# Kernel tuning notes

Measured on AMD Instinct MI355X. Metric: run time of the kernel, lower is better.

The kernel has to match this reference:

```python
import jax, jax.numpy as jnp
import numpy as np

N, C, H, W = 16, 64, 128, 128
SHIFT = 1  # frozen value of torch module's random.randint(-2, 2) drawn at __init__


def setup_inputs() -> dict:
    key = jax.random.key(0)
    k1, k2, k3 = jax.random.split(key, 3)
    x = jax.random.normal(k1, (N, C, H, W), dtype=jnp.float32)
    # p_3: Conv2d(c, c, (1,5), padding=(0,2), bias=False) -> weight (C_out, C_in, 1, 5)
    w3 = jax.random.normal(k2, (C, C, 1, 5), dtype=jnp.float32) * (1.0 / np.sqrt(5.0 * C))
    # p_7: Conv2d(9c, c, 1, groups=c, bias=False) -> per output channel, 9 input channels: (C, 9)
    w7 = jax.random.normal(k3, (C, 9), dtype=jnp.float32) * (1.0 / 3.0)
    return {"x": x, "w3": w3, "w7": w7}


def reference(x, w3, w7):
    n, c, h, w = x.shape
    # t_1: F.unfold(x, (1,3), dilation=(1,2), padding=(0,2)) -> width offsets -2, 0, +2 (zero padded)
    xp = jnp.pad(x, ((0, 0), (0, 0), (0, 0), (2, 2)))
    t1 = jnp.stack([xp[..., 0:w], xp[..., 2:w + 2], xp[..., 4:w + 4]], axis=2)  # (n,c,3,h,w)
    # t_3: 1x5 conv, padding (0,2)
    t3 = jax.lax.conv_general_dilated(
        x, w3, window_strides=(1, 1), padding=[(0, 0), (2, 2)],
        dimension_numbers=("NCHW", "OIHW", "NCHW"))  # (n,c,h,w)
    # t_4: F.unfold(t1 as (n,3c,h,w), (3,1), padding=(1,0)) -> height offsets -1, 0, +1
    t1p = jnp.pad(t1, ((0, 0), (0, 0), (0, 0), (1, 1), (0, 0)))
    t4 = jnp.stack([t1p[..., 0:h, :], t1p[..., 1:h + 1, :], t1p[..., 2:h + 2, :]],
                   axis=3)  # (n, c, 3[w_off], 3[h_off], h, w)
    # t_5: roll along the W axis (dim 5)
    t5 = jnp.roll(t4, SHIFT, axis=5)
    # t_6: maximum of lhs (n,c,1,3,h,w) and rhs (n,c,3,3,h,w); lhs offset dim aligns with rhs dim 3
    t6 = jnp.maximum(t1[:, :, None, :, :, :], t5)  # (n,c,3,3,h,w)
    # t_7: grouped 1x1 conv, groups=c, 9 input channels per group -> 1 output channel
    t6f = t6.reshape(n, c, 9, h, w)
    t7 = jnp.einsum("nckhw,ck->nchw", t6f, w7)
    return t7 * t3
```

## Files before the change

kernel.cpp:

```cpp
#include <hip/hip_runtime.h>

#define NN 16
#define CC 64
#define HH 128
#define WW 128

#define LDS_STRIDE 72
#define T3B_STRIDE 132

typedef __attribute__((ext_vector_type(8))) short short8;
typedef __attribute__((ext_vector_type(4))) float floatx4;

__device__ __forceinline__ short f2bf(float f) {
    union { float f; unsigned u; } v; v.f = f;
    unsigned r = v.u + 0x7fffu + ((v.u >> 16) & 1u);
    return (short)(r >> 16);
}
__device__ __forceinline__ unsigned pack2bf(float lo, float hi) {
    union { float f; unsigned u; } a, b; a.f = lo; b.f = hi;
    unsigned ra = a.u + 0x7fffu + ((a.u >> 16) & 1u);
    unsigned rb = b.u + 0x7fffu + ((b.u >> 16) & 1u);
    return (ra >> 16) | (rb & 0xffff0000u);
}
__device__ __forceinline__ float bf2f(unsigned short u) {
    union { unsigned u; float f; } v; v.u = ((unsigned)u) << 16;
    return v.f;
}

__global__ __launch_bounds__(256) void prep_w(const float* __restrict__ w3,
                                              short* __restrict__ Abf,
                                              float* __restrict__ zp) {
    int idx = blockIdx.x * 256 + threadIdx.x;
    if (idx < CC * CC * 5) {
        int tap = idx % 5;
        int ci  = (idx / 5) % CC;
        int co  = idx / (5 * CC);
        Abf[co * 320 + tap * 64 + ci] = f2bf(w3[idx]);
    }
    if (blockIdx.x == 0 && threadIdx.x < 64) zp[threadIdx.x] = 0.f;
}

__global__ __launch_bounds__(256, 4) void fused(const float* __restrict__ x,
                                                const short* __restrict__ Abf,
                                                const float* __restrict__ w7,
                                                const float* __restrict__ zp,
                                                float* __restrict__ out) {
    __shared__ __align__(16) char smem[132 * LDS_STRIDE * 2];
    short*    xsT = (short*)smem;
    unsigned* xsW = (unsigned*)smem;
    short*    t3b = (short*)smem;

    const int bid = blockIdx.x;
    const int nh  = ((bid & 7) << 8) | (bid >> 3);
    const int n   = nh >> 7;
    const int h   = nh & (HH - 1);
    const int tid = threadIdx.x;

    const float* xbase = x + (((size_t)n * CC) * HH + h) * WW;
    {
        const int cp  = tid & 31;
        const int wqg = tid >> 5;
        const float* r0 = xbase + (size_t)(2 * cp) * (HH * WW);
        const float* r1 = r0 + HH * WW;
        #pragma unroll
        for (int q = 0; q < 4; ++q) {
            int wq = wqg * 4 + q;
            float4 a = *(const float4*)(r0 + wq * 4);
            float4 b = *(const float4*)(r1 + wq * 4);
            int wp = wq * 4 + 2;
            xsW[(wp + 0) * 36 + cp] = pack2bf(a.x, b.x);
            xsW[(wp + 1) * 36 + cp] = pack2bf(a.y, b.y);
            xsW[(wp + 2) * 36 + cp] = pack2bf(a.z, b.z);
            xsW[(wp + 3) * 36 + cp] = pack2bf(a.w, b.w);
        }
        if (tid < 128) {
            int wpi = tid >> 5;
            int wpz = (wpi < 2) ? wpi : 128 + wpi;
            xsW[wpz * 36 + (tid & 31)] = 0u;
        }
    }
    __syncthreads();

    const int W    = tid >> 6;
    const int lane = tid & 63;
    const int lm   = lane & 15;
    const int g    = lane >> 4;

    floatx4 acc[8];
    #pragma unroll
    for (int nt = 0; nt < 8; ++nt) acc[nt] = (floatx4){0.f, 0.f, 0.f, 0.f};

    const short* arow = Abf + (W * 16 + lm) * 320;

    for (int ks = 0; ks < 10; ++ks) {
        const int kbase = ks * 32 + g * 8;
        const int tap   = kbase >> 6;
        const int cib   = kbase & 63;

        short8 a = *(const short8*)(arow + kbase);
        #pragma unroll
        for (int nt = 0; nt < 8; ++nt) {
            int wp = nt * 16 + lm + tap;
            short8 b = *(const short8*)&xsT[wp * LDS_STRIDE + cib];
            acc[nt] = __builtin_amdgcn_mfma_f32_16x16x32_bf16(a, b, acc[nt], 0, 0, 0);
        }
    }
    __syncthreads();

    #pragma unroll
    for (int nt = 0; nt < 8; ++nt) {
        #pragma unroll
        for (int r = 0; r < 4; ++r) {
            int co = W * 16 + g * 4 + r;
            t3b[co * T3B_STRIDE + nt * 16 + lm] = f2bf(acc[nt][r]);
        }
    }

    const int w0  = (tid & 31) * 4;
    const int chi = tid >> 5;
    const bool isw = (w0 == 0);
    const int src  = lane | 31;

    const float* p[9];
    int s[9];
    const float* xb0 = x + (((size_t)(n * CC + chi)) * HH) * WW;
    #pragma unroll
    for (int r = 0; r < 3; ++r) {
        int hh = h + r - 1;
        bool hok = (unsigned)hh < HH;
        #pragma unroll
        for (int q = 0; q < 3; ++q) {
            int cb = w0 - 4 + q * 4;
            bool ok = hok && (unsigned)cb < WW;
            p[r * 3 + q] = ok ? (xb0 + (size_t)hh * WW + cb) : zp;
            s[r * 3 + q] = ok ? (8 * HH * WW) : 0;
        }
    }
    const float* wcp = w7 + chi * 9;
    int t3o = chi * T3B_STRIDE + w0;
    float* outp = out + ((((size_t)(n * CC + chi)) * HH + h) * WW) + w0;

    float4 cur[9];
    #pragma unroll
    for (int t = 0; t < 9; ++t) { cur[t] = *(const float4*)p[t]; p[t] += s[t]; }

    __syncthreads();

    #pragma unroll
    for (int it = 0; it < 8; ++it) {
        float4 nxt[9];
        if (it < 7) {
            #pragma unroll
            for (int t = 0; t < 9; ++t) { nxt[t] = *(const float4*)p[t]; p[t] += s[t]; }
        }

        float win[3][12];
        #pragma unroll
        for (int r = 0; r < 3; ++r) {
            #pragma unroll
            for (int q = 0; q < 3; ++q) {
                float4 v = cur[r * 3 + q];
                win[r][q * 4 + 0] = v.x; win[r][q * 4 + 1] = v.y;
                win[r][q * 4 + 2] = v.z; win[r][q * 4 + 3] = v.w;
            }
        }
        float wrap0[3], wrap1[3];
        #pragma unroll
        for (int r = 0; r < 3; ++r) {
            wrap0[r] = __shfl(win[r][5], src);
            wrap1[r] = __shfl(win[r][7], src);
        }

        float wc[9];
        #pragma unroll
        for (int t = 0; t < 9; ++t) wc[t] = wcp[t];

        ushort4 tv = *(const ushort4*)&t3b[t3o];
        float t3v[4] = {bf2f(tv.x), bf2f(tv.y), bf2f(tv.z), bf2f(tv.w)};

        float res[4];
        #pragma unroll
        for (int e = 0; e < 4; ++e) {
            float a = 0.f;
            #pragma unroll
            for (int j = 0; j < 3; ++j) {
                #pragma unroll
                for (int i = 0; i < 3; ++i) {
                    float lhs = win[1][e + 2 * i + 2];
                    float rhs = win[i][e + 2 * j + 1];
                    if (e == 0)
                        rhs = isw ? ((j == 0) ? wrap0[i]
                                   : (j == 1) ? wrap1[i] : 0.f)
                                  : rhs;
                    a = fmaf(wc[j * 3 + i], fmaxf(lhs, rhs), a);
                }
            }
            res[e] = a;
        }
        float4 o;
        o.x = res[0] * t3v[0]; o.y = res[1] * t3v[1];
        o.z = res[2] * t3v[2]; o.w = res[3] * t3v[3];
        *(float4*)outp = o;

        wcp  += 8 * 9;
        t3o  += 8 * T3B_STRIDE;
        outp += (size_t)8 * HH * WW;
        #pragma unroll
        for (int t = 0; t < 9; ++t) cur[t] = nxt[t];
    }
}

extern "C" void kernel_launch(void* const* d_in, const int* in_sizes, int n_in,
                              void* d_out, int out_size, void* d_ws, size_t ws_size,
                              hipStream_t stream) {
    const float* x  = (const float*)d_in[0];
    const float* w3 = (const float*)d_in[1];
    const float* w7 = (const float*)d_in[2];
    float* out = (float*)d_out;

    short* Abf = (short*)d_ws;
    float* zp  = (float*)((char*)d_ws + 40960);

    prep_w<<<(CC * CC * 5 + 255) / 256, 256, 0, stream>>>(w3, Abf, zp);
    fused<<<NN * HH, 256, 0, stream>>>(x, Abf, w7, zp, out);
}
```

Measured before the change: 152.7 us.

## Retile MFMA to 32x64 per wave and overlap epilogue loads

Each wave now computes two 16-row output-channel tiles over half the width, rather than one 16-row tile over the full width. This halves the LDS B-operand reads per MFMA by reusing each B fragment for two A fragments. The t3 bf16 store to LDS is moved after the first global prefetch of x, with sched_barriers to keep that order. The w7/t3 loads are also hoisted ahead of the compute in each loop iteration. The cost is an extra A-fragment load per k-step from global memory, and the sched_barriers constrain the compiler's scheduling.

```diff
diff --git a/kernel.cpp b/kernel.cpp
--- a/kernel.cpp
+++ b/kernel.cpp
@@ -85,36 +85,33 @@
     const int lane = tid & 63;
     const int lm   = lane & 15;
     const int g    = lane >> 4;
-
-    floatx4 acc[8];
-    #pragma unroll
-    for (int nt = 0; nt < 8; ++nt) acc[nt] = (floatx4){0.f, 0.f, 0.f, 0.f};
-
-    const short* arow = Abf + (W * 16 + lm) * 320;
+    const int mh   = W >> 1;
+    const int wh   = W & 1;
+
+    floatx4 acc[2][4];
+    #pragma unroll
+    for (int m = 0; m < 2; ++m)
+        #pragma unroll
+        for (int j = 0; j < 4; ++j) acc[m][j] = (floatx4){0.f, 0.f, 0.f, 0.f};
+
+    const short* arow = Abf + (mh * 32 + lm) * 320;
 
     for (int ks = 0; ks < 10; ++ks) {
         const int kbase = ks * 32 + g * 8;
         const int tap   = kbase >> 6;
         const int cib   = kbase & 63;
 
-        short8 a = *(const short8*)(arow + kbase);
-        #pragma unroll
-        for (int nt = 0; nt < 8; ++nt) {
-            int wp = nt * 16 + lm + tap;
+        short8 a0 = *(const short8*)(arow + kbase);
+        short8 a1 = *(const short8*)(arow + 16 * 320 + kbase);
+        #pragma unroll
+        for (int j = 0; j < 4; ++j) {
+            int wp = (wh * 4 + j) * 16 + lm + tap;
             short8 b = *(const short8*)&xsT[wp * LDS_STRIDE + cib];
-            acc[nt] = __builtin_amdgcn_mfma_f32_16x16x32_bf16(a, b, acc[nt], 0, 0, 0);
+            acc[0][j] = __builtin_amdgcn_mfma_f32_16x16x32_bf16(a0, b, acc[0][j], 0, 0, 0);
+            acc[1][j] = __builtin_amdgcn_mfma_f32_16x16x32_bf16(a1, b, acc[1][j], 0, 0, 0);
         }
     }
     __syncthreads();
-
-    #pragma unroll
-    for (int nt = 0; nt < 8; ++nt) {
-        #pragma unroll
-        for (int r = 0; r < 4; ++r) {
-            int co = W * 16 + g * 4 + r;
-            t3b[co * T3B_STRIDE + nt * 16 + lm] = f2bf(acc[nt][r]);
-        }
-    }
 
     const int w0  = (tid & 31) * 4;
     const int chi = tid >> 5;
@@ -143,6 +140,17 @@
     float4 cur[9];
     #pragma unroll
     for (int t = 0; t < 9; ++t) { cur[t] = *(const float4*)p[t]; p[t] += s[t]; }
+    __builtin_amdgcn_sched_barrier(0);
+
+    #pragma unroll
+    for (int m = 0; m < 2; ++m)
+        #pragma unroll
+        for (int j = 0; j < 4; ++j)
+            #pragma unroll
+            for (int r = 0; r < 4; ++r) {
+                int co = (mh * 2 + m) * 16 + g * 4 + r;
+                t3b[co * T3B_STRIDE + (wh * 4 + j) * 16 + lm] = f2bf(acc[m][j][r]);
+            }
 
     __syncthreads();
 
@@ -153,6 +161,12 @@
             #pragma unroll
             for (int t = 0; t < 9; ++t) { nxt[t] = *(const float4*)p[t]; p[t] += s[t]; }
         }
+        float wc[9];
+        #pragma unroll
+        for (int t = 0; t < 9; ++t) wc[t] = wcp[t];
+        ushort4 tv = *(const ushort4*)&t3b[t3o];
+
+        __builtin_amdgcn_sched_barrier(0);
 
         float win[3][12];
         #pragma unroll
@@ -171,11 +185,6 @@
             wrap1[r] = __shfl(win[r][7], src);
         }
 
-        float wc[9];
-        #pragma unroll
-        for (int t = 0; t < 9; ++t) wc[t] = wcp[t];
-
-        ushort4 tv = *(const ushort4*)&t3b[t3o];
         float t3v[4] = {bf2f(tv.x), bf2f(tv.y), bf2f(tv.z), bf2f(tv.w)};
 
         float res[4];
```

Result: slower. 158.3 us (+3.6%).
